# Kernel tuning notes

Hardware: AMD Instinct MI355X
Metric: run time of the kernel (lower is better)

Reference implementation:

```python
import jax, jax.numpy as jnp
import numpy as np

VOCAB, EMBED, UNITS, B, T = 1024, 512, 1024, 64, 512


def _lstm_layer(x, W, U, b):
    """Keras LSTMCell semantics: gates ordered [i, f, g, o], sigmoid recurrent
    activation, tanh activation. x: [B, T, D]; W: [D, 4U]; U: [U, 4U]; b: [4U]."""
    Bsz = x.shape[0]
    units = U.shape[0]
    # Precompute input contribution for all timesteps (one big GEMM).
    xz = jnp.einsum('btd,dg->btg', x, W) + b  # [B, T, 4U]

    def step(carry, xz_t):
        h, c = carry
        z = xz_t + h @ U  # [B, 4U]
        i, f, g, o = jnp.split(z, 4, axis=-1)
        i = jax.nn.sigmoid(i)
        f = jax.nn.sigmoid(f)
        g = jnp.tanh(g)
        o = jax.nn.sigmoid(o)
        c = f * c + i * g
        h = o * jnp.tanh(c)
        return (h, c), h

    init = (jnp.zeros((Bsz, units), x.dtype), jnp.zeros((Bsz, units), x.dtype))
    (h, c), hs = jax.lax.scan(step, init, jnp.swapaxes(xz, 0, 1))  # scan over T
    return jnp.swapaxes(hs, 0, 1), h, c  # [B, T, U], [B, U], [B, U]


def setup_inputs() -> dict:
    key = jax.random.key(0)
    ks = jax.random.split(key, 8)
    s_e = 1.0 / np.sqrt(EMBED)
    s_u = 1.0 / np.sqrt(UNITS)
    return {
        'tokens': jax.random.randint(ks[0], (B, T), 0, VOCAB, dtype=jnp.int32),
        'embed_table': jax.random.normal(ks[1], (VOCAB, EMBED), jnp.float32) * 0.05,
        'W0': jax.random.normal(ks[2], (EMBED, 4 * UNITS), jnp.float32) * s_e,
        'U0': jax.random.normal(ks[3], (UNITS, 4 * UNITS), jnp.float32) * s_u,
        'b0': jnp.zeros((4 * UNITS,), jnp.float32),
        'W1': jax.random.normal(ks[4], (UNITS, 4 * UNITS), jnp.float32) * s_u,
        'U1': jax.random.normal(ks[5], (UNITS, 4 * UNITS), jnp.float32) * s_u,
        'b1': jnp.zeros((4 * UNITS,), jnp.float32),
    }


def reference(tokens, embed_table, W0, U0, b0, W1, U1, b1):
    # Embedding lookup (dropout is identity at inference / rate handled outside).
    x = embed_table[tokens]  # [B, T, EMBED]
    x, h0, c0 = _lstm_layer(x, W0, U0, b0)
    out, h1, c1 = _lstm_layer(x, W1, U1, b1)
    return out  # [B, T, UNITS]
```

## Files before the change

### kernel.cpp

```cpp
#include <hip/hip_runtime.h>
#include <math.h>

typedef __attribute__((ext_vector_type(8))) short s8v;
typedef __attribute__((ext_vector_type(4))) float f4v;
typedef unsigned long long u64;

#define TT 512
#define UU 1024
#define HSZ 65536u

#define B_TZ   0ull
#define B_A0H  16777216ull
#define B_A0L  25165824ull
#define B_A1H  33554432ull
#define B_A1L  50331648ull
#define B_H0   67108864ull
#define B_H1   (B_H0 + 3ull*HSZ*4ull)
#define B_BAR  (B_H1 + 3ull*HSZ*4ull)

__device__ __forceinline__ unsigned short f2bf(float x) {
  unsigned u = __float_as_uint(x);
  return (unsigned short)((u + 0x7fffu + ((u >> 16) & 1u)) >> 16);
}

#define MFMA(a, b, c) __builtin_amdgcn_mfma_f32_16x16x32_bf16((a), (b), (c), 0, 0, 0)

__device__ __forceinline__ u64 ldsc(const u64* p) {
  return __hip_atomic_load(p, __ATOMIC_RELAXED, __HIP_MEMORY_SCOPE_AGENT);
}
__device__ __forceinline__ void stsc(u64* p, u64 v) {
  __hip_atomic_store(p, v, __ATOMIC_RELAXED, __HIP_MEMORY_SCOPE_AGENT);
}

__device__ __forceinline__ float sigm(float x) {
  return __builtin_amdgcn_rcpf(1.f + __expf(-x));
}
__device__ __forceinline__ float tanha(float x) {
  return 1.f - 2.f * __builtin_amdgcn_rcpf(1.f + __expf(x + x));
}

__device__ __forceinline__ void unpack8q(const u64* q, s8v& bh, s8v& bl) {
  union { uint4 u; s8v s; } H, L;
  H.u.x = __builtin_amdgcn_perm((unsigned)(q[0] >> 32), (unsigned)q[0], 0x07060302u);
  H.u.y = __builtin_amdgcn_perm((unsigned)(q[1] >> 32), (unsigned)q[1], 0x07060302u);
  H.u.z = __builtin_amdgcn_perm((unsigned)(q[2] >> 32), (unsigned)q[2], 0x07060302u);
  H.u.w = __builtin_amdgcn_perm((unsigned)(q[3] >> 32), (unsigned)q[3], 0x07060302u);
  L.u.x = __builtin_amdgcn_perm((unsigned)(q[0] >> 32), (unsigned)q[0], 0x05040100u);
  L.u.y = __builtin_amdgcn_perm((unsigned)(q[1] >> 32), (unsigned)q[1], 0x05040100u);
  L.u.z = __builtin_amdgcn_perm((unsigned)(q[2] >> 32), (unsigned)q[2], 0x05040100u);
  L.u.w = __builtin_amdgcn_perm((unsigned)(q[3] >> 32), (unsigned)q[3], 0x05040100u);
  bh = H.s; bl = L.s;
}

__global__ __launch_bounds__(256) void pack_a0_k(const float* __restrict__ U0,
                                                 unsigned short* __restrict__ A0h,
                                                 unsigned short* __restrict__ A0l) {
  unsigned e = blockIdx.x * 256u + threadIdx.x;
  unsigned j = e & 7u, lane = (e >> 3) & 63u, ch = (e >> 9) & 3u;
  unsigned wv = (e >> 11) & 7u, wg = e >> 14;
  unsigned quad = lane >> 4, col = lane & 15u;
  unsigned k = wv * 128u + ch * 32u + quad * 8u + j;
  unsigned c = (col & 3u) * 1024u + wg * 4u + (col >> 2);
  float x = U0[(size_t)k * 4096u + c];
  unsigned short h = f2bf(x);
  A0h[e] = h;
  A0l[e] = f2bf(x - __uint_as_float(((unsigned)h) << 16));
}

__global__ __launch_bounds__(256) void pack_a1_k(const float* __restrict__ W1,
                                                 const float* __restrict__ U1,
                                                 unsigned short* __restrict__ A1h,
                                                 unsigned short* __restrict__ A1l) {
  unsigned e = blockIdx.x * 256u + threadIdx.x;
  unsigned j = e & 7u, lane = (e >> 3) & 63u, ch = (e >> 9) & 7u;
  unsigned wv = (e >> 12) & 7u, wg = e >> 15;
  unsigned quad = lane >> 4, col = lane & 15u;
  unsigned k = wv * 128u + (ch & 3u) * 32u + quad * 8u + j;
  unsigned c = (col & 3u) * 1024u + wg * 4u + (col >> 2);
  float x = (ch < 4u) ? W1[(size_t)k * 4096u + c] : U1[(size_t)k * 4096u + c];
  unsigned short h = f2bf(x);
  A1h[e] = h;
  A1l[e] = f2bf(x - __uint_as_float(((unsigned)h) << 16));
}

__global__ __launch_bounds__(256) void tz_gemm_k(const float* __restrict__ embed,
                                                 const float* __restrict__ W0,
                                                 const float* __restrict__ b0,
                                                 float* __restrict__ tz) {
  const int c0 = blockIdx.x << 6;
  const int v0 = blockIdx.y << 6;
  __shared__ float As[32][65];
  __shared__ float Bs[32][65];
  const int tid = threadIdx.x;
  const int tr = tid >> 4, tc = tid & 15;
  float acc[4][4];
#pragma unroll
  for (int r = 0; r < 4; ++r)
#pragma unroll
    for (int c = 0; c < 4; ++c) acc[r][c] = 0.f;

  for (int kc = 0; kc < 512; kc += 32) {
    __syncthreads();
    {
      int kk = tid & 31, vv = tid >> 5;
#pragma unroll
      for (int p = 0; p < 8; ++p)
        As[kk][vv + (p << 3)] = embed[(size_t)(v0 + vv + (p << 3)) * 512 + kc + kk];
    }
    {
      int cc = tid & 63, kk = tid >> 6;
#pragma unroll
      for (int p = 0; p < 8; ++p)
        Bs[kk + (p << 2)][cc] = W0[(size_t)(kc + kk + (p << 2)) * 4096 + c0 + cc];
    }
    __syncthreads();
#pragma unroll 8
    for (int kk = 0; kk < 32; ++kk) {
      float av[4], bv[4];
#pragma unroll
      for (int r = 0; r < 4; ++r) av[r] = As[kk][(tr << 2) + r];
#pragma unroll
      for (int c = 0; c < 4; ++c) bv[c] = Bs[kk][(tc << 2) + c];
#pragma unroll
      for (int r = 0; r < 4; ++r)
#pragma unroll
        for (int c = 0; c < 4; ++c) acc[r][c] = fmaf(av[r], bv[c], acc[r][c]);
    }
  }
#pragma unroll
  for (int r = 0; r < 4; ++r) {
    int v = v0 + (tr << 2) + r;
#pragma unroll
    for (int c = 0; c < 4; ++c) {
      int col = c0 + (tc << 2) + c;
      int g = col >> 10, u = col & 1023;
      tz[(size_t)v * 4096 + (u << 2) + g] = acc[r][c] + b0[col];
    }
  }
}

__device__ __forceinline__ void arrive(unsigned* xc, unsigned* gc, unsigned* gen, int grp) {
  unsigned old = __hip_atomic_fetch_add(xc + grp * 32, 1u, __ATOMIC_RELAXED,
                                        __HIP_MEMORY_SCOPE_AGENT);
  if ((old & 31u) == 31u) {
    unsigned o2 = __hip_atomic_fetch_add(gc, 1u, __ATOMIC_RELAXED, __HIP_MEMORY_SCOPE_AGENT);
    if ((o2 & 7u) == 7u)
      __hip_atomic_store(gen, (o2 >> 3) + 1u, __ATOMIC_RELAXED, __HIP_MEMORY_SCOPE_AGENT);
  }
}
__device__ __forceinline__ void waitgen(unsigned* gen, unsigned target) {
  while (__hip_atomic_load(gen, __ATOMIC_RELAXED, __HIP_MEMORY_SCOPE_AGENT) < target)
    __builtin_amdgcn_s_sleep(1);
}

__global__ __launch_bounds__(512) void lstm_coop_k(const int* __restrict__ tokens,
                                                   const float* __restrict__ tz,
                                                   const unsigned short* __restrict__ A0h,
                                                   const unsigned short* __restrict__ A0l,
                                                   const unsigned short* __restrict__ A1h,
                                                   const unsigned short* __restrict__ A1l,
                                                   const float* __restrict__ b1,
                                                   unsigned* __restrict__ h0w,
                                                   unsigned* __restrict__ h1w,
                                                   float* __restrict__ out,
                                                   unsigned* __restrict__ bar) {
  __shared__ float zpf[4 * 2080];
  __shared__ unsigned hx[64 * 5];

  const int tid = threadIdx.x;
  const int wg = blockIdx.x;
  const int lane = tid & 63;
  const int wv = __builtin_amdgcn_readfirstlane(tid >> 6);
  const int quad = lane >> 4, n = lane & 15;
  const int j = tid >> 6;
  const int grp = wg & 7;
  const bool bt = (tid == 448);

  unsigned* xcA = bar;        unsigned* xcB = bar + 256;
  unsigned* gcA = bar + 512;  unsigned* gcB = bar + 544;
  unsigned* genA = bar + 576; unsigned* genB = bar + 608;

  s8v a0h[4], a0l[4], a1h[8], a1l[8];
  {
    const s8v* p0h = (const s8v*)A0h + ((wg * 8 + wv) * 4) * 64 + lane;
    const s8v* p0l = (const s8v*)A0l + ((wg * 8 + wv) * 4) * 64 + lane;
#pragma unroll
    for (int ch = 0; ch < 4; ++ch) { a0h[ch] = p0h[ch * 64]; a0l[ch] = p0l[ch * 64]; }
    const s8v* p1h = (const s8v*)A1h + ((wg * 8 + wv) * 8) * 64 + lane;
    const s8v* p1l = (const s8v*)A1l + ((wg * 8 + wv) * 8) * 64 + lane;
#pragma unroll
    for (int ch = 0; ch < 8; ++ch) { a1h[ch] = p1h[ch * 64]; a1l[ch] = p1l[ch * 64]; }
  }

  float c0 = 0.f, c1 = 0.f, hout = 0.f;
  f4v b1v = {0.f, 0.f, 0.f, 0.f};
  if (tid < 256) {
    b1v.x = b1[0 * 1024 + wg * 4 + j];
    b1v.y = b1[1 * 1024 + wg * 4 + j];
    b1v.z = b1[2 * 1024 + wg * 4 + j];
    b1v.w = b1[3 * 1024 + wg * 4 + j];
  }

  const unsigned pcb = ((unsigned)(wg >> 3) << 11) + ((unsigned)(wg & 1) << 8) +
                       ((unsigned)((wg >> 1) & 3) << 6) + ((unsigned)(lane >> 4) << 9) +
                       ((unsigned)(lane & 15) << 2);

  for (int ss = 0; ss <= TT; ++ss) {
    const int s0w = ss % 3, s0r = (ss + 2) % 3;
    const int s1wr = (ss + 2) % 3, s1r = (ss + 1) % 3;

    if (bt) waitgen(genA, (unsigned)ss);
    __syncthreads();

    f4v tzv = {0.f, 0.f, 0.f, 0.f};
    if (ss < TT && tid < 256) {
      int tok = tokens[lane * TT + ss];
      tzv = ((const f4v*)tz)[(size_t)tok * 1024 + (wg << 2) + j];
    }
    f4v acc0[4], acc1[4];
#pragma unroll
    for (int t = 0; t < 4; ++t) { acc0[t] = (f4v){0,0,0,0}; acc1[t] = (f4v){0,0,0,0}; }
    {
      const u64* hb = (const u64*)(h0w + s0r * HSZ);
#pragma unroll
      for (int ch = 0; ch < 4; ++ch) {
        const u64* p = hb + (((wv << 2) + ch) << 10) + (lane << 1);
        u64 q[4][4];
#pragma unroll
        for (int t = 0; t < 4; ++t) {
          q[t][0] = ldsc(p + (t << 8));
          q[t][1] = ldsc(p + (t << 8) + 1);
          q[t][2] = ldsc(p + (t << 8) + 128);
          q[t][3] = ldsc(p + (t << 8) + 129);
        }
#pragma unroll
        for (int t = 0; t < 4; ++t) {
          s8v bh, bl; unpack8q(q[t], bh, bl);
          acc0[t] = MFMA(a0h[ch], bh, acc0[t]);
          acc1[t] = MFMA(a1h[ch], bh, acc1[t]);
          acc0[t] = MFMA(a0l[ch], bh, acc0[t]);
          acc1[t] = MFMA(a1l[ch], bh, acc1[t]);
          acc0[t] = MFMA(a0h[ch], bl, acc0[t]);
          acc1[t] = MFMA(a1h[ch], bl, acc1[t]);
        }
      }
    }

    if (ss < TT) {
#pragma unroll
      for (int t = 0; t < 4; ++t)
#pragma unroll
        for (int r = 0; r < 4; ++r)
          zpf[r * 2080 + quad * 520 + (wv << 6) + t * 16 + n] = acc0[t][r];
      __syncthreads();
      if (tid < 256) {
        f4v s = tzv;
#pragma unroll
        for (int g = 0; g < 4; ++g) {
          float x = 0.f;
#pragma unroll
          for (int w = 0; w < 8; ++w) x += zpf[g * 2080 + j * 520 + (w << 6) + lane];
          s[g] += x;
        }
        float iG = sigm(s.x);
        float fG = sigm(s.y);
        float gG = tanha(s.z);
        float oG = sigm(s.w);
        c0 = fG * c0 + iG * gG;
        float h = oG * tanha(c0);
        unsigned hb16 = (unsigned)f2bf(h);
        unsigned lo16 = (unsigned)f2bf(h - __uint_as_float(hb16 << 16));
        hx[lane * 5 + j] = (hb16 << 16) | lo16;
      }
      __syncthreads();
      if (wv == 7) {
        unsigned v0 = hx[lane * 5 + 0], v1 = hx[lane * 5 + 1];
        unsigned v2 = hx[lane * 5 + 2], v3 = hx[lane * 5 + 3];
        u64* p = (u64*)(h0w + s0w * HSZ + pcb);
        stsc(p, (u64)v0 | ((u64)v1 << 32));
        stsc(p + 1, (u64)v2 | ((u64)v3 << 32));
        asm volatile("s_waitcnt vmcnt(0)" ::: "memory");
        if (lane == 0) arrive(xcA, gcA, genA, grp);
      }
    }

    if (bt && ss >= 1) waitgen(genB, (unsigned)(ss - 1));
    __syncthreads();

    if (ss >= 1) {
      {
        const u64* hb = (const u64*)(h1w + s1r * HSZ);
#pragma unroll
        for (int ch = 0; ch < 4; ++ch) {
          const u64* p = hb + (((wv << 2) + ch) << 10) + (lane << 1);
          u64 q[4][4];
#pragma unroll
          for (int t = 0; t < 4; ++t) {
            q[t][0] = ldsc(p + (t << 8));
            q[t][1] = ldsc(p + (t << 8) + 1);
            q[t][2] = ldsc(p + (t << 8) + 128);
            q[t][3] = ldsc(p + (t << 8) + 129);
          }
#pragma unroll
          for (int t = 0; t < 4; ++t) {
            s8v bh, bl; unpack8q(q[t], bh, bl);
            acc1[t] = MFMA(a1h[4 + ch], bh, acc1[t]);
            acc1[t] = MFMA(a1l[4 + ch], bh, acc1[t]);
            acc1[t] = MFMA(a1h[4 + ch], bl, acc1[t]);
          }
        }
      }
#pragma unroll
      for (int t = 0; t < 4; ++t)
#pragma unroll
        for (int r = 0; r < 4; ++r)
          zpf[r * 2080 + quad * 520 + (wv << 6) + t * 16 + n] = acc1[t][r];
      __syncthreads();
      if (tid < 256) {
        f4v s = b1v;
#pragma unroll
        for (int g = 0; g < 4; ++g) {
          float x = 0.f;
#pragma unroll
          for (int w = 0; w < 8; ++w) x += zpf[g * 2080 + j * 520 + (w << 6) + lane];
          s[g] += x;
        }
        float iG = sigm(s.x);
        float fG = sigm(s.y);
        float gG = tanha(s.z);
        float oG = sigm(s.w);
        c1 = fG * c1 + iG * gG;
        hout = oG * tanha(c1);
        unsigned hb16 = (unsigned)f2bf(hout);
        unsigned lo16 = (unsigned)f2bf(hout - __uint_as_float(hb16 << 16));
        hx[lane * 5 + j] = (hb16 << 16) | lo16;
      }
      __syncthreads();
      if (wv == 7) {
        unsigned v0 = hx[lane * 5 + 0], v1 = hx[lane * 5 + 1];
        unsigned v2 = hx[lane * 5 + 2], v3 = hx[lane * 5 + 3];
        u64* p = (u64*)(h1w + s1wr * HSZ + pcb);
        stsc(p, (u64)v0 | ((u64)v1 << 32));
        stsc(p + 1, (u64)v2 | ((u64)v3 << 32));
        asm volatile("s_waitcnt vmcnt(0)" ::: "memory");
        if (lane == 0) arrive(xcB, gcB, genB, grp);
      }
      if (tid < 256)
        out[(size_t)lane * (TT * UU) + (size_t)(ss - 1) * UU + (wg << 2) + j] = hout;
    }
  }
}

extern "C" void kernel_launch(void* const* d_in, const int* in_sizes, int n_in,
                              void* d_out, int out_size, void* d_ws, size_t ws_size,
                              hipStream_t stream) {
  const int*   tokens = (const int*)d_in[0];
  const float* embed  = (const float*)d_in[1];
  const float* W0     = (const float*)d_in[2];
  const float* U0     = (const float*)d_in[3];
  const float* b0     = (const float*)d_in[4];
  const float* W1     = (const float*)d_in[5];
  const float* U1     = (const float*)d_in[6];
  const float* b1     = (const float*)d_in[7];
  char* ws = (char*)d_ws;
  float*          tz  = (float*)(ws + B_TZ);
  unsigned short* A0h = (unsigned short*)(ws + B_A0H);
  unsigned short* A0l = (unsigned short*)(ws + B_A0L);
  unsigned short* A1h = (unsigned short*)(ws + B_A1H);
  unsigned short* A1l = (unsigned short*)(ws + B_A1L);
  unsigned*       h0w = (unsigned*)(ws + B_H0);
  unsigned*       h1w = (unsigned*)(ws + B_H1);
  unsigned*       bar = (unsigned*)(ws + B_BAR);
  float* out = (float*)d_out;

  hipMemsetAsync(ws + B_H0, 0, (size_t)(6ull * HSZ * 4ull + 4096ull), stream);

  pack_a0_k<<<16384, 256, 0, stream>>>(U0, A0h, A0l);
  pack_a1_k<<<32768, 256, 0, stream>>>(W1, U1, A1h, A1l);
  tz_gemm_k<<<dim3(64, 16), 256, 0, stream>>>(embed, W0, b0, tz);

  void* args[] = {(void*)&tokens, (void*)&tz, (void*)&A0h, (void*)&A0l,
                  (void*)&A1h, (void*)&A1l, (void*)&b1, (void*)&h0w, (void*)&h1w,
                  (void*)&out, (void*)&bar};
  hipLaunchCooperativeKernel((void*)lstm_coop_k, dim3(256), dim3(512), args, 0, stream);
}
```

Before: 7.209 ms.

## Split batch into two independent halves with separate barriers to overlap recurrence

Splits the 64-sequence batch into two halves of 32, each with its own hidden-state buffers and grid-barrier counters, and processes layer-0 A, layer-0 B, layer-1 A, layer-1 B as four phases per timestep. The goal is that while one half waits on its global barrier the other half's work is already published, hiding barrier latency behind useful compute. It doubles the number of barrier waits and __syncthreads per step, and each phase does half-sized MFMA tiles, so fixed per-phase overhead may dominate.

```diff
diff --git a/kernel.cpp b/kernel.cpp
--- a/kernel.cpp
+++ b/kernel.cpp
@@ -7,16 +7,15 @@
 
 #define TT 512
 #define UU 1024
-#define HSZ 65536u
+#define HHALF 32768u
 
 #define B_TZ   0ull
 #define B_A0H  16777216ull
 #define B_A0L  25165824ull
 #define B_A1H  33554432ull
 #define B_A1L  50331648ull
-#define B_H0   67108864ull
-#define B_H1   (B_H0 + 3ull*HSZ*4ull)
-#define B_BAR  (B_H1 + 3ull*HSZ*4ull)
+#define B_H    67108864ull
+#define B_BAR  (B_H + 12ull*HHALF*4ull)
 
 __device__ __forceinline__ unsigned short f2bf(float x) {
   unsigned u = __float_as_uint(x);
@@ -139,13 +138,15 @@
   }
 }
 
-__device__ __forceinline__ void arrive(unsigned* xc, unsigned* gc, unsigned* gen, int grp) {
-  unsigned old = __hip_atomic_fetch_add(xc + grp * 32, 1u, __ATOMIC_RELAXED,
+__device__ __forceinline__ void arrive(unsigned* cb, int grp) {
+  unsigned old = __hip_atomic_fetch_add(cb + grp * 32, 1u, __ATOMIC_RELAXED,
                                         __HIP_MEMORY_SCOPE_AGENT);
   if ((old & 31u) == 31u) {
-    unsigned o2 = __hip_atomic_fetch_add(gc, 1u, __ATOMIC_RELAXED, __HIP_MEMORY_SCOPE_AGENT);
+    unsigned o2 = __hip_atomic_fetch_add(cb + 512, 1u, __ATOMIC_RELAXED,
+                                         __HIP_MEMORY_SCOPE_AGENT);
     if ((o2 & 7u) == 7u)
-      __hip_atomic_store(gen, (o2 >> 3) + 1u, __ATOMIC_RELAXED, __HIP_MEMORY_SCOPE_AGENT);
+      __hip_atomic_store(cb + 576, (o2 >> 3) + 1u, __ATOMIC_RELAXED,
+                         __HIP_MEMORY_SCOPE_AGENT);
   }
 }
 __device__ __forceinline__ void waitgen(unsigned* gen, unsigned target) {
@@ -160,25 +161,30 @@
                                                    const unsigned short* __restrict__ A1h,
                                                    const unsigned short* __restrict__ A1l,
                                                    const float* __restrict__ b1,
-                                                   unsigned* __restrict__ h0w,
-                                                   unsigned* __restrict__ h1w,
+                                                   unsigned* __restrict__ hbase,
                                                    float* __restrict__ out,
                                                    unsigned* __restrict__ bar) {
-  __shared__ float zpf[4 * 2080];
-  __shared__ unsigned hx[64 * 5];
+  __shared__ float zpf[4224];
+  __shared__ unsigned hx[160];
 
   const int tid = threadIdx.x;
   const int wg = blockIdx.x;
   const int lane = tid & 63;
   const int wv = __builtin_amdgcn_readfirstlane(tid >> 6);
   const int quad = lane >> 4, n = lane & 15;
-  const int j = tid >> 6;
+  const int uj = tid >> 5;
+  const int ub = tid & 31;
   const int grp = wg & 7;
-  const bool bt = (tid == 448);
-
-  unsigned* xcA = bar;        unsigned* xcB = bar + 256;
-  unsigned* gcA = bar + 512;  unsigned* gcB = bar + 544;
-  unsigned* genA = bar + 576; unsigned* genB = bar + 608;
+  const bool bt = (tid == 0);
+
+  unsigned* h0A = hbase;
+  unsigned* h0B = hbase + 3 * HHALF;
+  unsigned* h1A = hbase + 6 * HHALF;
+  unsigned* h1B = hbase + 9 * HHALF;
+  unsigned* cbA0 = bar;
+  unsigned* cbB0 = bar + 1024;
+  unsigned* cbA1 = bar + 2048;
+  unsigned* cbB1 = bar + 3072;
 
   s8v a0h[4], a0l[4], a1h[8], a1l[8];
   {
@@ -192,161 +198,149 @@
     for (int ch = 0; ch < 8; ++ch) { a1h[ch] = p1h[ch * 64]; a1l[ch] = p1l[ch * 64]; }
   }
 
-  float c0 = 0.f, c1 = 0.f, hout = 0.f;
+  float cs0A = 0.f, cs0B = 0.f, cs1A = 0.f, cs1B = 0.f;
   f4v b1v = {0.f, 0.f, 0.f, 0.f};
-  if (tid < 256) {
-    b1v.x = b1[0 * 1024 + wg * 4 + j];
-    b1v.y = b1[1 * 1024 + wg * 4 + j];
-    b1v.z = b1[2 * 1024 + wg * 4 + j];
-    b1v.w = b1[3 * 1024 + wg * 4 + j];
-  }
-
-  const unsigned pcb = ((unsigned)(wg >> 3) << 11) + ((unsigned)(wg & 1) << 8) +
-                       ((unsigned)((wg >> 1) & 3) << 6) + ((unsigned)(lane >> 4) << 9) +
-                       ((unsigned)(lane & 15) << 2);
+  if (tid < 128) {
+    b1v.x = b1[0 * 1024 + wg * 4 + uj];
+    b1v.y = b1[1 * 1024 + wg * 4 + uj];
+    b1v.z = b1[2 * 1024 + wg * 4 + uj];
+    b1v.w = b1[3 * 1024 + wg * 4 + uj];
+  }
+
+  const unsigned pcbb = ((unsigned)(wg >> 3) << 10) + ((unsigned)(wg & 1) << 8) +
+                        (((unsigned)(wg >> 1) & 3u) << 6);
+
+  auto l0 = [&](const unsigned* hs, f4v* acc0, f4v* accw) {
+    const u64* hb = (const u64*)hs;
+#pragma unroll
+    for (int ch = 0; ch < 4; ++ch) {
+      const u64* p = hb + (((wv << 2) + ch) << 9) + (lane << 1);
+      u64 q[2][4];
+#pragma unroll
+      for (int t = 0; t < 2; ++t) {
+        q[t][0] = ldsc(p + (t << 8));
+        q[t][1] = ldsc(p + (t << 8) + 1);
+        q[t][2] = ldsc(p + (t << 8) + 128);
+        q[t][3] = ldsc(p + (t << 8) + 129);
+      }
+#pragma unroll
+      for (int t = 0; t < 2; ++t) {
+        s8v bh, bl; unpack8q(q[t], bh, bl);
+        acc0[t] = MFMA(a0h[ch], bh, acc0[t]);
+        accw[t] = MFMA(a1h[ch], bh, accw[t]);
+        acc0[t] = MFMA(a0l[ch], bh, acc0[t]);
+        accw[t] = MFMA(a1l[ch], bh, accw[t]);
+        acc0[t] = MFMA(a0h[ch], bl, acc0[t]);
+        accw[t] = MFMA(a1h[ch], bl, accw[t]);
+      }
+    }
+  };
+
+  auto l1 = [&](const unsigned* hs, f4v* acc) {
+    const u64* hb = (const u64*)hs;
+#pragma unroll
+    for (int ch = 0; ch < 4; ++ch) {
+      const u64* p = hb + (((wv << 2) + ch) << 9) + (lane << 1);
+      u64 q[2][4];
+#pragma unroll
+      for (int t = 0; t < 2; ++t) {
+        q[t][0] = ldsc(p + (t << 8));
+        q[t][1] = ldsc(p + (t << 8) + 1);
+        q[t][2] = ldsc(p + (t << 8) + 128);
+        q[t][3] = ldsc(p + (t << 8) + 129);
+      }
+#pragma unroll
+      for (int t = 0; t < 2; ++t) {
+        s8v bh, bl; unpack8q(q[t], bh, bl);
+        acc[t] = MFMA(a1h[4 + ch], bh, acc[t]);
+        acc[t] = MFMA(a1l[4 + ch], bh, acc[t]);
+        acc[t] = MFMA(a1h[4 + ch], bl, acc[t]);
+      }
+    }
+  };
+
+  auto tail = [&](f4v* acc, f4v bias, float& cst, unsigned* hslot, unsigned* cb) -> float {
+#pragma unroll
+    for (int t = 0; t < 2; ++t)
+#pragma unroll
+      for (int r = 0; r < 4; ++r)
+        zpf[r * 1056 + quad * 264 + (wv << 5) + t * 16 + n] = acc[t][r];
+    __syncthreads();
+    float ho = 0.f;
+    if (tid < 128) {
+      f4v s = bias;
+#pragma unroll
+      for (int g = 0; g < 4; ++g) {
+        float x = 0.f;
+#pragma unroll
+        for (int w = 0; w < 8; ++w) x += zpf[g * 1056 + uj * 264 + (w << 5) + ub];
+        s[g] += x;
+      }
+      float iG = sigm(s.x);
+      float fG = sigm(s.y);
+      float gG = tanha(s.z);
+      float oG = sigm(s.w);
+      cst = fG * cst + iG * gG;
+      ho = oG * tanha(cst);
+      unsigned hb16 = (unsigned)f2bf(ho);
+      unsigned lo16 = (unsigned)f2bf(ho - __uint_as_float(hb16 << 16));
+      hx[ub * 5 + uj] = (hb16 << 16) | lo16;
+    }
+    __syncthreads();
+    if (wv == 7) {
+      int b = lane >> 1, pr = lane & 1;
+      unsigned v0 = hx[b * 5 + pr * 2];
+      unsigned v1 = hx[b * 5 + pr * 2 + 1];
+      u64* p = (u64*)(hslot + pcbb + ((b >> 4) << 9) + ((b & 15) << 2) + (pr << 1));
+      stsc(p, (u64)v0 | ((u64)v1 << 32));
+      asm volatile("s_waitcnt vmcnt(0)" ::: "memory");
+      if (lane == 0) arrive(cb, grp);
+    }
+    return ho;
+  };
 
   for (int ss = 0; ss <= TT; ++ss) {
     const int s0w = ss % 3, s0r = (ss + 2) % 3;
-    const int s1wr = (ss + 2) % 3, s1r = (ss + 1) % 3;
-
-    if (bt) waitgen(genA, (unsigned)ss);
-    __syncthreads();
-
-    f4v tzv = {0.f, 0.f, 0.f, 0.f};
-    if (ss < TT && tid < 256) {
-      int tok = tokens[lane * TT + ss];
-      tzv = ((const f4v*)tz)[(size_t)tok * 1024 + (wg << 2) + j];
-    }
-    f4v acc0[4], acc1[4];
-#pragma unroll
-    for (int t = 0; t < 4; ++t) { acc0[t] = (f4v){0,0,0,0}; acc1[t] = (f4v){0,0,0,0}; }
-    {
-      const u64* hb = (const u64*)(h0w + s0r * HSZ);
-#pragma unroll
-      for (int ch = 0; ch < 4; ++ch) {
-        const u64* p = hb + (((wv << 2) + ch) << 10) + (lane << 1);
-        u64 q[4][4];
-#pragma unroll
-        for (int t = 0; t < 4; ++t) {
-          q[t][0] = ldsc(p + (t << 8));
-          q[t][1] = ldsc(p + (t << 8) + 1);
-          q[t][2] = ldsc(p + (t << 8) + 128);
-          q[t][3] = ldsc(p + (t << 8) + 129);
-        }
-#pragma unroll
-        for (int t = 0; t < 4; ++t) {
-          s8v bh, bl; unpack8q(q[t], bh, bl);
-          acc0[t] = MFMA(a0h[ch], bh, acc0[t]);
-          acc1[t] = MFMA(a1h[ch], bh, acc1[t]);
-          acc0[t] = MFMA(a0l[ch], bh, acc0[t]);
-          acc1[t] = MFMA(a1l[ch], bh, acc1[t]);
-          acc0[t] = MFMA(a0h[ch], bl, acc0[t]);
-          acc1[t] = MFMA(a1h[ch], bl, acc1[t]);
-        }
-      }
-    }
-
-    if (ss < TT) {
-#pragma unroll
-      for (int t = 0; t < 4; ++t)
-#pragma unroll
-        for (int r = 0; r < 4; ++r)
-          zpf[r * 2080 + quad * 520 + (wv << 6) + t * 16 + n] = acc0[t][r];
-      __syncthreads();
-      if (tid < 256) {
-        f4v s = tzv;
-#pragma unroll
-        for (int g = 0; g < 4; ++g) {
-          float x = 0.f;
-#pragma unroll
-          for (int w = 0; w < 8; ++w) x += zpf[g * 2080 + j * 520 + (w << 6) + lane];
-          s[g] += x;
-        }
-        float iG = sigm(s.x);
-        float fG = sigm(s.y);
-        float gG = tanha(s.z);
-        float oG = sigm(s.w);
-        c0 = fG * c0 + iG * gG;
-        float h = oG * tanha(c0);
-        unsigned hb16 = (unsigned)f2bf(h);
-        unsigned lo16 = (unsigned)f2bf(h - __uint_as_float(hb16 << 16));
-        hx[lane * 5 + j] = (hb16 << 16) | lo16;
-      }
-      __syncthreads();
-      if (wv == 7) {
-        unsigned v0 = hx[lane * 5 + 0], v1 = hx[lane * 5 + 1];
-        unsigned v2 = hx[lane * 5 + 2], v3 = hx[lane * 5 + 3];
-        u64* p = (u64*)(h0w + s0w * HSZ + pcb);
-        stsc(p, (u64)v0 | ((u64)v1 << 32));
-        stsc(p + 1, (u64)v2 | ((u64)v3 << 32));
-        asm volatile("s_waitcnt vmcnt(0)" ::: "memory");
-        if (lane == 0) arrive(xcA, gcA, genA, grp);
-      }
-    }
-
-    if (bt && ss >= 1) waitgen(genB, (unsigned)(ss - 1));
-    __syncthreads();
-
+    const int s1w = (ss + 2) % 3, s1r = (ss + 1) % 3;
+
+    f4v tzvA = {0.f, 0.f, 0.f, 0.f}, tzvB = {0.f, 0.f, 0.f, 0.f};
+    if (ss < TT && tid < 128) {
+      tzvA = ((const f4v*)tz)[(size_t)tokens[ub * TT + ss] * 1024 + (wg << 2) + uj];
+      tzvB = ((const f4v*)tz)[(size_t)tokens[(ub + 32) * TT + ss] * 1024 + (wg << 2) + uj];
+    }
+
+    if (bt) waitgen(cbA0 + 576, (unsigned)ss);
+    __syncthreads();
+    f4v acc0[2], w1A[2];
+#pragma unroll
+    for (int t = 0; t < 2; ++t) { acc0[t] = (f4v){0,0,0,0}; w1A[t] = (f4v){0,0,0,0}; }
+    l0(h0A + s0r * HHALF, acc0, w1A);
+    if (ss < TT) (void)tail(acc0, tzvA, cs0A, h0A + s0w * HHALF, cbA0);
+
+    if (bt) waitgen(cbB0 + 576, (unsigned)ss);
+    __syncthreads();
+    f4v acc0b[2], w1B[2];
+#pragma unroll
+    for (int t = 0; t < 2; ++t) { acc0b[t] = (f4v){0,0,0,0}; w1B[t] = (f4v){0,0,0,0}; }
+    l0(h0B + s0r * HHALF, acc0b, w1B);
+    if (ss < TT) (void)tail(acc0b, tzvB, cs0B, h0B + s0w * HHALF, cbB0);
+
+    if (bt && ss >= 1) waitgen(cbA1 + 576, (unsigned)(ss - 1));
+    __syncthreads();
     if (ss >= 1) {
-      {
-        const u64* hb = (const u64*)(h1w + s1r * HSZ);
-#pragma unroll
-        for (int ch = 0; ch < 4; ++ch) {
-          const u64* p = hb + (((wv << 2) + ch) << 10) + (lane << 1);
-          u64 q[4][4];
-#pragma unroll
-          for (int t = 0; t < 4; ++t) {
-            q[t][0] = ldsc(p + (t << 8));
-            q[t][1] = ldsc(p + (t << 8) + 1);
-            q[t][2] = ldsc(p + (t << 8) + 128);
-            q[t][3] = ldsc(p + (t << 8) + 129);
-          }
-#pragma unroll
-          for (int t = 0; t < 4; ++t) {
-            s8v bh, bl; unpack8q(q[t], bh, bl);
-            acc1[t] = MFMA(a1h[4 + ch], bh, acc1[t]);
-            acc1[t] = MFMA(a1l[4 + ch], bh, acc1[t]);
-            acc1[t] = MFMA(a1h[4 + ch], bl, acc1[t]);
-          }
-        }
-      }
-#pragma unroll
-      for (int t = 0; t < 4; ++t)
-#pragma unroll
-        for (int r = 0; r < 4; ++r)
-          zpf[r * 2080 + quad * 520 + (wv << 6) + t * 16 + n] = acc1[t][r];
-      __syncthreads();
-      if (tid < 256) {
-        f4v s = b1v;
-#pragma unroll
-        for (int g = 0; g < 4; ++g) {
-          float x = 0.f;
-#pragma unroll
-          for (int w = 0; w < 8; ++w) x += zpf[g * 2080 + j * 520 + (w << 6) + lane];
-          s[g] += x;
-        }
-        float iG = sigm(s.x);
-        float fG = sigm(s.y);
-        float gG = tanha(s.z);
-        float oG = sigm(s.w);
-        c1 = fG * c1 + iG * gG;
-        hout = oG * tanha(c1);
-        unsigned hb16 = (unsigned)f2bf(hout);
-        unsigned lo16 = (unsigned)f2bf(hout - __uint_as_float(hb16 << 16));
-        hx[lane * 5 + j] = (hb16 << 16) | lo16;
-      }
-      __syncthreads();
-      if (wv == 7) {
-        unsigned v0 = hx[lane * 5 + 0], v1 = hx[lane * 5 + 1];
-        unsigned v2 = hx[lane * 5 + 2], v3 = hx[lane * 5 + 3];
-        u64* p = (u64*)(h1w + s1wr * HSZ + pcb);
-        stsc(p, (u64)v0 | ((u64)v1 << 32));
-        stsc(p + 1, (u64)v2 | ((u64)v3 << 32));
-        asm volatile("s_waitcnt vmcnt(0)" ::: "memory");
-        if (lane == 0) arrive(xcB, gcB, genB, grp);
-      }
-      if (tid < 256)
-        out[(size_t)lane * (TT * UU) + (size_t)(ss - 1) * UU + (wg << 2) + j] = hout;
+      l1(h1A + s1r * HHALF, w1A);
+      float ho = tail(w1A, b1v, cs1A, h1A + s1w * HHALF, cbA1);
+      if (tid < 128)
+        out[(size_t)ub * (TT * UU) + (size_t)(ss - 1) * UU + (wg << 2) + uj] = ho;
+    }
+
+    if (bt && ss >= 1) waitgen(cbB1 + 576, (unsigned)(ss - 1));
+    __syncthreads();
+    if (ss >= 1) {
+      l1(h1B + s1r * HHALF, w1B);
+      float ho = tail(w1B, b1v, cs1B, h1B + s1w * HHALF, cbB1);
+      if (tid < 128)
+        out[(size_t)(ub + 32) * (TT * UU) + (size_t)(ss - 1) * UU + (wg << 2) + uj] = ho;
     }
   }
 }
@@ -368,19 +362,18 @@
   unsigned short* A0l = (unsigned short*)(ws + B_A0L);
   unsigned short* A1h = (unsigned short*)(ws + B_A1H);
   unsigned short* A1l = (unsigned short*)(ws + B_A1L);
-  unsigned*       h0w = (unsigned*)(ws + B_H0);
-  unsigned*       h1w = (unsigned*)(ws + B_H1);
+  unsigned*       hb  = (unsigned*)(ws + B_H);
   unsigned*       bar = (unsigned*)(ws + B_BAR);
   float* out = (float*)d_out;
 
-  hipMemsetAsync(ws + B_H0, 0, (size_t)(6ull * HSZ * 4ull + 4096ull), stream);
+  hipMemsetAsync(ws + B_H, 0, (size_t)(12ull * HHALF * 4ull + 16384ull), stream);
 
   pack_a0_k<<<16384, 256, 0, stream>>>(U0, A0h, A0l);
   pack_a1_k<<<32768, 256, 0, stream>>>(W1, U1, A1h, A1l);
   tz_gemm_k<<<dim3(64, 16), 256, 0, stream>>>(embed, W0, b0, tz);
 
   void* args[] = {(void*)&tokens, (void*)&tz, (void*)&A0h, (void*)&A0l,
-                  (void*)&A1h, (void*)&A1l, (void*)&b1, (void*)&h0w, (void*)&h1w,
+                  (void*)&A1h, (void*)&A1l, (void*)&b1, (void*)&hb,
                   (void*)&out, (void*)&bar};
   hipLaunchCooperativeKernel((void*)lstm_coop_k, dim3(256), dim3(512), args, 0, stream);
 }
```

After: 8.279 ms. +14.8%, slower.

## Restructure LSTM step sync: per-wave generation polling and fewer block barriers

Applied to the files above, without the earlier changes.

Replaces the single-thread generation wait plus block barrier with every wave polling its own replicated generation flag, and the grid barrier now counts per-wave arrivals (64 per group) and fans the generation out to 8 padded slots. Gate math and h stores move to dedicated waves (4-5 for layer 0, 6-7 for layer 1) that write h directly without staging through shared memory, removing one __syncthreads per layer. The LDS reduction buffer is double-buffered and padded (stride 65) to reduce bank conflicts, and the output is stored as float2. The intent is to shorten the per-timestep critical path of the two recurrent layers, at the cost of more atomic polling traffic and extra flag stores.

```diff
diff --git a/kernel.cpp b/kernel.cpp
--- a/kernel.cpp
+++ b/kernel.cpp
@@ -139,18 +139,25 @@
   }
 }
 
-__device__ __forceinline__ void arrive(unsigned* xc, unsigned* gc, unsigned* gen, int grp) {
-  unsigned old = __hip_atomic_fetch_add(xc + grp * 32, 1u, __ATOMIC_RELAXED,
+__device__ __forceinline__ void arrive2(unsigned* cb, int grp) {
+  unsigned old = __hip_atomic_fetch_add(cb + grp * 32, 1u, __ATOMIC_RELAXED,
                                         __HIP_MEMORY_SCOPE_AGENT);
-  if ((old & 31u) == 31u) {
-    unsigned o2 = __hip_atomic_fetch_add(gc, 1u, __ATOMIC_RELAXED, __HIP_MEMORY_SCOPE_AGENT);
-    if ((o2 & 7u) == 7u)
-      __hip_atomic_store(gen, (o2 >> 3) + 1u, __ATOMIC_RELAXED, __HIP_MEMORY_SCOPE_AGENT);
-  }
-}
-__device__ __forceinline__ void waitgen(unsigned* gen, unsigned target) {
-  while (__hip_atomic_load(gen, __ATOMIC_RELAXED, __HIP_MEMORY_SCOPE_AGENT) < target)
-    __builtin_amdgcn_s_sleep(1);
+  if ((old & 63u) == 63u) {
+    unsigned o2 = __hip_atomic_fetch_add(cb + 512, 1u, __ATOMIC_RELAXED,
+                                         __HIP_MEMORY_SCOPE_AGENT);
+    if ((o2 & 7u) == 7u) {
+      unsigned g = (o2 >> 3) + 1u;
+#pragma unroll
+      for (int k = 0; k < 8; ++k)
+        __hip_atomic_store(cb + 576 + k * 16, g, __ATOMIC_RELAXED,
+                           __HIP_MEMORY_SCOPE_AGENT);
+    }
+  }
+}
+__device__ __forceinline__ void pollgen(const unsigned* g, unsigned target) {
+  while (__hip_atomic_load(g, __ATOMIC_RELAXED, __HIP_MEMORY_SCOPE_AGENT) < target)
+    __builtin_amdgcn_s_sleep(2);
+  __builtin_amdgcn_sched_barrier(0);
 }
 
 __global__ __launch_bounds__(512) void lstm_coop_k(const int* __restrict__ tokens,
@@ -164,21 +171,18 @@
                                                    unsigned* __restrict__ h1w,
                                                    float* __restrict__ out,
                                                    unsigned* __restrict__ bar) {
-  __shared__ float zpf[4 * 2080];
-  __shared__ unsigned hx[64 * 5];
+  __shared__ float zpf[2][8320];
 
   const int tid = threadIdx.x;
   const int wg = blockIdx.x;
   const int lane = tid & 63;
   const int wv = __builtin_amdgcn_readfirstlane(tid >> 6);
   const int quad = lane >> 4, n = lane & 15;
-  const int j = tid >> 6;
   const int grp = wg & 7;
-  const bool bt = (tid == 448);
-
-  unsigned* xcA = bar;        unsigned* xcB = bar + 256;
-  unsigned* gcA = bar + 512;  unsigned* gcB = bar + 544;
-  unsigned* genA = bar + 576; unsigned* genB = bar + 608;
+  const int j0 = (wv & 1) << 1;
+
+  unsigned* cbA = bar;
+  unsigned* cbB = bar + 1024;
 
   s8v a0h[4], a0l[4], a1h[8], a1l[8];
   {
@@ -192,161 +196,171 @@
     for (int ch = 0; ch < 8; ++ch) { a1h[ch] = p1h[ch * 64]; a1l[ch] = p1l[ch * 64]; }
   }
 
-  float c0 = 0.f, c1 = 0.f, hout = 0.f;
-  f4v b1v = {0.f, 0.f, 0.f, 0.f};
-  if (tid < 256) {
-    b1v.x = b1[0 * 1024 + wg * 4 + j];
-    b1v.y = b1[1 * 1024 + wg * 4 + j];
-    b1v.z = b1[2 * 1024 + wg * 4 + j];
-    b1v.w = b1[3 * 1024 + wg * 4 + j];
-  }
-
-  const unsigned pcb = ((unsigned)(wg >> 3) << 11) + ((unsigned)(wg & 1) << 8) +
-                       ((unsigned)((wg >> 1) & 3) << 6) + ((unsigned)(lane >> 4) << 9) +
-                       ((unsigned)(lane & 15) << 2);
+  float cA0 = 0.f, cB0 = 0.f, cA1 = 0.f, cB1 = 0.f;
+  f4v b1v0 = {0.f, 0.f, 0.f, 0.f}, b1v1 = {0.f, 0.f, 0.f, 0.f};
+  if (wv >= 6) {
+    b1v0.x = b1[0 * 1024 + wg * 4 + j0];
+    b1v0.y = b1[1 * 1024 + wg * 4 + j0];
+    b1v0.z = b1[2 * 1024 + wg * 4 + j0];
+    b1v0.w = b1[3 * 1024 + wg * 4 + j0];
+    b1v1.x = b1[0 * 1024 + wg * 4 + j0 + 1];
+    b1v1.y = b1[1 * 1024 + wg * 4 + j0 + 1];
+    b1v1.z = b1[2 * 1024 + wg * 4 + j0 + 1];
+    b1v1.w = b1[3 * 1024 + wg * 4 + j0 + 1];
+  }
+
+  const unsigned pcbu = ((unsigned)(wg >> 3) << 11) + ((unsigned)(wg & 1) << 8) +
+                        (((unsigned)(wg >> 1) & 3u) << 6) + ((unsigned)(lane >> 4) << 9) +
+                        ((unsigned)(lane & 15) << 2);
+
+  auto l0 = [&](const unsigned* hs, f4v* acc0, f4v* accw) {
+    const u64* hb = (const u64*)hs;
+#pragma unroll
+    for (int ch = 0; ch < 4; ++ch) {
+      const u64* p = hb + (((wv << 2) + ch) << 10) + (lane << 1);
+      u64 q[4][4];
+#pragma unroll
+      for (int t = 0; t < 4; ++t) {
+        q[t][0] = ldsc(p + (t << 8));
+        q[t][1] = ldsc(p + (t << 8) + 1);
+        q[t][2] = ldsc(p + (t << 8) + 128);
+        q[t][3] = ldsc(p + (t << 8) + 129);
+      }
+#pragma unroll
+      for (int t = 0; t < 4; ++t) {
+        s8v bh, bl; unpack8q(q[t], bh, bl);
+        acc0[t] = MFMA(a0h[ch], bh, acc0[t]);
+        accw[t] = MFMA(a1h[ch], bh, accw[t]);
+        acc0[t] = MFMA(a0l[ch], bh, acc0[t]);
+        accw[t] = MFMA(a1l[ch], bh, accw[t]);
+        acc0[t] = MFMA(a0h[ch], bl, acc0[t]);
+        accw[t] = MFMA(a1h[ch], bl, accw[t]);
+      }
+    }
+  };
+  auto l1 = [&](const unsigned* hs, f4v* acc) {
+    const u64* hb = (const u64*)hs;
+#pragma unroll
+    for (int ch = 0; ch < 4; ++ch) {
+      const u64* p = hb + (((wv << 2) + ch) << 10) + (lane << 1);
+      u64 q[4][4];
+#pragma unroll
+      for (int t = 0; t < 4; ++t) {
+        q[t][0] = ldsc(p + (t << 8));
+        q[t][1] = ldsc(p + (t << 8) + 1);
+        q[t][2] = ldsc(p + (t << 8) + 128);
+        q[t][3] = ldsc(p + (t << 8) + 129);
+      }
+#pragma unroll
+      for (int t = 0; t < 4; ++t) {
+        s8v bh, bl; unpack8q(q[t], bh, bl);
+        acc[t] = MFMA(a1h[4 + ch], bh, acc[t]);
+        acc[t] = MFMA(a1l[4 + ch], bh, acc[t]);
+        acc[t] = MFMA(a1h[4 + ch], bl, acc[t]);
+      }
+    }
+  };
 
   for (int ss = 0; ss <= TT; ++ss) {
     const int s0w = ss % 3, s0r = (ss + 2) % 3;
-    const int s1wr = (ss + 2) % 3, s1r = (ss + 1) % 3;
-
-    if (bt) waitgen(genA, (unsigned)ss);
+    const int s1w = (ss + 2) % 3, s1r = (ss + 1) % 3;
+
+    f4v tz0 = {0.f, 0.f, 0.f, 0.f}, tz1 = {0.f, 0.f, 0.f, 0.f};
+    if ((wv == 4 || wv == 5) && ss < TT) {
+      size_t base = (size_t)tokens[lane * TT + ss] * 1024 + (wg << 2);
+      tz0 = ((const f4v*)tz)[base + j0];
+      tz1 = ((const f4v*)tz)[base + j0 + 1];
+    }
+
+    pollgen(cbA + 576 + wv * 16, (unsigned)ss);
+    f4v acc0[4], accw[4];
+#pragma unroll
+    for (int t = 0; t < 4; ++t) { acc0[t] = (f4v){0,0,0,0}; accw[t] = (f4v){0,0,0,0}; }
+    l0(h0w + s0r * HSZ, acc0, accw);
+#pragma unroll
+    for (int t = 0; t < 4; ++t)
+#pragma unroll
+      for (int r = 0; r < 4; ++r)
+        zpf[0][r * 2080 + quad * 520 + wv * 65 + t * 16 + n] = acc0[t][r];
     __syncthreads();
 
-    f4v tzv = {0.f, 0.f, 0.f, 0.f};
-    if (ss < TT && tid < 256) {
-      int tok = tokens[lane * TT + ss];
-      tzv = ((const f4v*)tz)[(size_t)tok * 1024 + (wg << 2) + j];
-    }
-    f4v acc0[4], acc1[4];
-#pragma unroll
-    for (int t = 0; t < 4; ++t) { acc0[t] = (f4v){0,0,0,0}; acc1[t] = (f4v){0,0,0,0}; }
-    {
-      const u64* hb = (const u64*)(h0w + s0r * HSZ);
-#pragma unroll
-      for (int ch = 0; ch < 4; ++ch) {
-        const u64* p = hb + (((wv << 2) + ch) << 10) + (lane << 1);
-        u64 q[4][4];
-#pragma unroll
-        for (int t = 0; t < 4; ++t) {
-          q[t][0] = ldsc(p + (t << 8));
-          q[t][1] = ldsc(p + (t << 8) + 1);
-          q[t][2] = ldsc(p + (t << 8) + 128);
-          q[t][3] = ldsc(p + (t << 8) + 129);
+    if (ss < TT && (wv == 4 || wv == 5)) {
+      f4v s0 = tz0, s1 = tz1;
+      const float* zb = zpf[0];
+#pragma unroll
+      for (int g = 0; g < 4; ++g) {
+        float x0 = 0.f, x1 = 0.f;
+#pragma unroll
+        for (int w = 0; w < 8; ++w) {
+          x0 += zb[g * 2080 + j0 * 520 + w * 65 + lane];
+          x1 += zb[g * 2080 + (j0 + 1) * 520 + w * 65 + lane];
         }
-#pragma unroll
-        for (int t = 0; t < 4; ++t) {
-          s8v bh, bl; unpack8q(q[t], bh, bl);
-          acc0[t] = MFMA(a0h[ch], bh, acc0[t]);
-          acc1[t] = MFMA(a1h[ch], bh, acc1[t]);
-          acc0[t] = MFMA(a0l[ch], bh, acc0[t]);
-          acc1[t] = MFMA(a1l[ch], bh, acc1[t]);
-          acc0[t] = MFMA(a0h[ch], bl, acc0[t]);
-          acc1[t] = MFMA(a1h[ch], bl, acc1[t]);
+        s0[g] += x0; s1[g] += x1;
+      }
+      float hA, hB;
+      {
+        float iG = sigm(s0.x), fG = sigm(s0.y), gG = tanha(s0.z), oG = sigm(s0.w);
+        cA0 = fG * cA0 + iG * gG; hA = oG * tanha(cA0);
+      }
+      {
+        float iG = sigm(s1.x), fG = sigm(s1.y), gG = tanha(s1.z), oG = sigm(s1.w);
+        cB0 = fG * cB0 + iG * gG; hB = oG * tanha(cB0);
+      }
+      unsigned hiA = (unsigned)f2bf(hA);
+      unsigned pA = (hiA << 16) | (unsigned)f2bf(hA - __uint_as_float(hiA << 16));
+      unsigned hiB = (unsigned)f2bf(hB);
+      unsigned pB = (hiB << 16) | (unsigned)f2bf(hB - __uint_as_float(hiB << 16));
+      u64* p = (u64*)(h0w + s0w * HSZ) + (pcbu >> 1) + (wv & 1);
+      stsc(p, (u64)pA | ((u64)pB << 32));
+      asm volatile("s_waitcnt vmcnt(0)" ::: "memory");
+      if (lane == 0) arrive2(cbA, grp);
+    }
+
+    if (ss >= 1) {
+      pollgen(cbB + 576 + wv * 16, (unsigned)(ss - 1));
+      l1(h1w + s1r * HSZ, accw);
+#pragma unroll
+      for (int t = 0; t < 4; ++t)
+#pragma unroll
+        for (int r = 0; r < 4; ++r)
+          zpf[1][r * 2080 + quad * 520 + wv * 65 + t * 16 + n] = accw[t][r];
+      __syncthreads();
+
+      if (wv >= 6) {
+        f4v s0 = b1v0, s1 = b1v1;
+        const float* zb = zpf[1];
+#pragma unroll
+        for (int g = 0; g < 4; ++g) {
+          float x0 = 0.f, x1 = 0.f;
+#pragma unroll
+          for (int w = 0; w < 8; ++w) {
+            x0 += zb[g * 2080 + j0 * 520 + w * 65 + lane];
+            x1 += zb[g * 2080 + (j0 + 1) * 520 + w * 65 + lane];
+          }
+          s0[g] += x0; s1[g] += x1;
         }
-      }
-    }
-
-    if (ss < TT) {
-#pragma unroll
-      for (int t = 0; t < 4; ++t)
-#pragma unroll
-        for (int r = 0; r < 4; ++r)
-          zpf[r * 2080 + quad * 520 + (wv << 6) + t * 16 + n] = acc0[t][r];
+        float hA, hB;
+        {
+          float iG = sigm(s0.x), fG = sigm(s0.y), gG = tanha(s0.z), oG = sigm(s0.w);
+          cA1 = fG * cA1 + iG * gG; hA = oG * tanha(cA1);
+        }
+        {
+          float iG = sigm(s1.x), fG = sigm(s1.y), gG = tanha(s1.z), oG = sigm(s1.w);
+          cB1 = fG * cB1 + iG * gG; hB = oG * tanha(cB1);
+        }
+        unsigned hiA = (unsigned)f2bf(hA);
+        unsigned pA = (hiA << 16) | (unsigned)f2bf(hA - __uint_as_float(hiA << 16));
+        unsigned hiB = (unsigned)f2bf(hB);
+        unsigned pB = (hiB << 16) | (unsigned)f2bf(hB - __uint_as_float(hiB << 16));
+        u64* p = (u64*)(h1w + s1w * HSZ) + (pcbu >> 1) + (wv & 1);
+        stsc(p, (u64)pA | ((u64)pB << 32));
+        asm volatile("s_waitcnt vmcnt(0)" ::: "memory");
+        if (lane == 0) arrive2(cbB, grp);
+        float2 ov; ov.x = hA; ov.y = hB;
+        *(float2*)&out[(size_t)lane * (TT * UU) + (size_t)(ss - 1) * UU + (wg << 2) + j0] = ov;
+      }
+    } else {
       __syncthreads();
-      if (tid < 256) {
-        f4v s = tzv;
-#pragma unroll
-        for (int g = 0; g < 4; ++g) {
-          float x = 0.f;
-#pragma unroll
-          for (int w = 0; w < 8; ++w) x += zpf[g * 2080 + j * 520 + (w << 6) + lane];
-          s[g] += x;
-        }
-        float iG = sigm(s.x);
-        float fG = sigm(s.y);
-        float gG = tanha(s.z);
-        float oG = sigm(s.w);
-        c0 = fG * c0 + iG * gG;
-        float h = oG * tanha(c0);
-        unsigned hb16 = (unsigned)f2bf(h);
-        unsigned lo16 = (unsigned)f2bf(h - __uint_as_float(hb16 << 16));
-        hx[lane * 5 + j] = (hb16 << 16) | lo16;
-      }
-      __syncthreads();
-      if (wv == 7) {
-        unsigned v0 = hx[lane * 5 + 0], v1 = hx[lane * 5 + 1];
-        unsigned v2 = hx[lane * 5 + 2], v3 = hx[lane * 5 + 3];
-        u64* p = (u64*)(h0w + s0w * HSZ + pcb);
-        stsc(p, (u64)v0 | ((u64)v1 << 32));
-        stsc(p + 1, (u64)v2 | ((u64)v3 << 32));
-        asm volatile("s_waitcnt vmcnt(0)" ::: "memory");
-        if (lane == 0) arrive(xcA, gcA, genA, grp);
-      }
-    }
-
-    if (bt && ss >= 1) waitgen(genB, (unsigned)(ss - 1));
-    __syncthreads();
-
-    if (ss >= 1) {
-      {
-        const u64* hb = (const u64*)(h1w + s1r * HSZ);
-#pragma unroll
-        for (int ch = 0; ch < 4; ++ch) {
-          const u64* p = hb + (((wv << 2) + ch) << 10) + (lane << 1);
-          u64 q[4][4];
-#pragma unroll
-          for (int t = 0; t < 4; ++t) {
-            q[t][0] = ldsc(p + (t << 8));
-            q[t][1] = ldsc(p + (t << 8) + 1);
-            q[t][2] = ldsc(p + (t << 8) + 128);
-            q[t][3] = ldsc(p + (t << 8) + 129);
-          }
-#pragma unroll
-          for (int t = 0; t < 4; ++t) {
-            s8v bh, bl; unpack8q(q[t], bh, bl);
-            acc1[t] = MFMA(a1h[4 + ch], bh, acc1[t]);
-            acc1[t] = MFMA(a1l[4 + ch], bh, acc1[t]);
-            acc1[t] = MFMA(a1h[4 + ch], bl, acc1[t]);
-          }
-        }
-      }
-#pragma unroll
-      for (int t = 0; t < 4; ++t)
-#pragma unroll
-        for (int r = 0; r < 4; ++r)
-          zpf[r * 2080 + quad * 520 + (wv << 6) + t * 16 + n] = acc1[t][r];
-      __syncthreads();
-      if (tid < 256) {
-        f4v s = b1v;
-#pragma unroll
-        for (int g = 0; g < 4; ++g) {
-          float x = 0.f;
-#pragma unroll
-          for (int w = 0; w < 8; ++w) x += zpf[g * 2080 + j * 520 + (w << 6) + lane];
-          s[g] += x;
-        }
-        float iG = sigm(s.x);
-        float fG = sigm(s.y);
-        float gG = tanha(s.z);
-        float oG = sigm(s.w);
-        c1 = fG * c1 + iG * gG;
-        hout = oG * tanha(c1);
-        unsigned hb16 = (unsigned)f2bf(hout);
-        unsigned lo16 = (unsigned)f2bf(hout - __uint_as_float(hb16 << 16));
-        hx[lane * 5 + j] = (hb16 << 16) | lo16;
-      }
-      __syncthreads();
-      if (wv == 7) {
-        unsigned v0 = hx[lane * 5 + 0], v1 = hx[lane * 5 + 1];
-        unsigned v2 = hx[lane * 5 + 2], v3 = hx[lane * 5 + 3];
-        u64* p = (u64*)(h1w + s1wr * HSZ + pcb);
-        stsc(p, (u64)v0 | ((u64)v1 << 32));
-        stsc(p + 1, (u64)v2 | ((u64)v3 << 32));
-        asm volatile("s_waitcnt vmcnt(0)" ::: "memory");
-        if (lane == 0) arrive(xcB, gcB, genB, grp);
-      }
-      if (tid < 256)
-        out[(size_t)lane * (TT * UU) + (size_t)(ss - 1) * UU + (wg << 2) + j] = hout;
     }
   }
 }
@@ -373,7 +387,7 @@
   unsigned*       bar = (unsigned*)(ws + B_BAR);
   float* out = (float*)d_out;
 
-  hipMemsetAsync(ws + B_H0, 0, (size_t)(6ull * HSZ * 4ull + 4096ull), stream);
+  hipMemsetAsync(ws + B_H0, 0, (size_t)(6ull * HSZ * 4ull + 16384ull), stream);
 
   pack_a0_k<<<16384, 256, 0, stream>>>(U0, A0h, A0l);
   pack_a1_k<<<32768, 256, 0, stream>>>(W1, U1, A1h, A1l);
```

Measured after the change: 6.576 ms. -8.8%, faster.
